# Optimization experiments

Hardware: AMD Instinct MI355X
Metric: run time of the kernel (lower is better)

## Reference

```python
import jax, jax.numpy as jnp
import numpy as np

N, E, D = 50000, 800000, 128   # nodes, edges, input feat dim
H, C = 4, 32                   # heads, per-head channels (H*C = 128)
OUT = 128                      # final linear out_channels
NEG_SLOPE = 0.2


def _glorot(k, shape):
    fan = shape[0] + shape[-1]
    return jax.random.normal(k, shape, jnp.float32) * np.float32(np.sqrt(2.0 / fan))


def setup_inputs() -> dict:
    key = jax.random.key(0)
    ks = jax.random.split(key, 16)
    HC = H * C
    z = lambda n: jnp.zeros((n,), jnp.float32)
    return {
        "x": jax.random.normal(ks[0], (N, D), jnp.float32),
        "edge_index": jax.random.randint(ks[1], (2, E), 0, N),
        "edge_attr": jax.random.uniform(ks[2], (E, 1), jnp.float32),
        # GATv2 layer 1 (in = D)
        "Wl1": _glorot(ks[3], (D, HC)), "bl1": z(HC),
        "Wr1": _glorot(ks[4], (D, HC)), "br1": z(HC),
        "We1": _glorot(ks[5], (1, HC)),
        "att1": _glorot(ks[6], (H, C)),
        "bo1": z(HC),
        # GATv2 layer 2 (in = H*C)
        "Wl2": _glorot(ks[7], (HC, HC)), "bl2": z(HC),
        "Wr2": _glorot(ks[8], (HC, HC)), "br2": z(HC),
        "We2": _glorot(ks[9], (1, HC)),
        "att2": _glorot(ks[10], (H, C)),
        "bo2": z(HC),
        # final Linear
        "Wlin": _glorot(ks[11], (HC, OUT)), "blin": z(OUT),
    }


def _segment_softmax(logits, seg, n):
    # logits: [E_tot, H], seg: [E_tot] target node ids
    m = jax.ops.segment_max(logits, seg, num_segments=n)          # [N, H]
    m = jnp.where(jnp.isfinite(m), m, 0.0)                         # empty-segment guard
    e = jnp.exp(logits - m[seg])
    s = jax.ops.segment_sum(e, seg, num_segments=n)                # [N, H]
    return e / (s[seg] + 1e-16)


def _gatv2_layer(x, src, dst, eattr, Wl, bl, Wr, br, We, att, bo):
    n = x.shape[0]
    xl = (x @ Wl + bl).reshape(n, H, C)   # source transform (lin_l)
    xr = (x @ Wr + br).reshape(n, H, C)   # target transform (lin_r)
    ee = (eattr @ We).reshape(-1, H, C)   # edge transform (lin_edge)
    m = jax.nn.leaky_relu(xl[src] + xr[dst] + ee, NEG_SLOPE)       # [E_tot, H, C]
    logits = jnp.einsum('ehc,hc->eh', m, att)                      # [E_tot, H]
    alpha = _segment_softmax(logits, dst, n)                       # [E_tot, H]
    out = jax.ops.segment_sum(xl[src] * alpha[..., None], dst, num_segments=n)
    return out.reshape(n, H * C) + bo


def _with_self_loops(edge_index, edge_attr, n):
    # PyG add_self_loops(fill_value='mean'): loop attr = mean of incoming edge attrs
    src, dst = edge_index[0], edge_index[1]
    sums = jax.ops.segment_sum(edge_attr, dst, num_segments=n)     # [N, 1]
    cnts = jax.ops.segment_sum(jnp.ones((edge_attr.shape[0], 1), edge_attr.dtype),
                               dst, num_segments=n)
    loop_attr = jnp.where(cnts > 0, sums / jnp.maximum(cnts, 1.0), 0.0)
    ar = jnp.arange(n, dtype=src.dtype)
    full_src = jnp.concatenate([src, ar])
    full_dst = jnp.concatenate([dst, ar])
    full_attr = jnp.concatenate([edge_attr, loop_attr], axis=0)
    return full_src, full_dst, full_attr


def reference(x, edge_index, edge_attr,
              Wl1, bl1, Wr1, br1, We1, att1, bo1,
              Wl2, bl2, Wr2, br2, We2, att2, bo2,
              Wlin, blin):
    x = x.astype(jnp.float32)
    edge_attr = edge_attr.astype(jnp.float32)
    src, dst, eattr = _with_self_loops(edge_index, edge_attr, x.shape[0])
    h = jax.nn.relu(_gatv2_layer(x, src, dst, eattr, Wl1, bl1, Wr1, br1, We1, att1, bo1))
    h = jax.nn.relu(_gatv2_layer(h, src, dst, eattr, Wl2, bl2, Wr2, br2, We2, att2, bo2))
    return jax.nn.relu(h @ Wlin + blin)
```

## Files before the change

kernel.cpp:

```cpp
#include <hip/hip_runtime.h>
#include <hip/hip_fp16.h>
#include <math.h>

#define NEG 0.2f
#define ROWS 48

typedef _Float16 hf2 __attribute__((ext_vector_type(2)));
typedef _Float16 hf8 __attribute__((ext_vector_type(8)));
typedef float f4 __attribute__((ext_vector_type(4)));

template <int CTRL>
__device__ __forceinline__ float dpp_radd(float x) {
  int t = __builtin_amdgcn_update_dpp(0, __float_as_int(x), CTRL, 0xf, 0xf,
                                      false);
  return x + __int_as_float(t);
}

__device__ __forceinline__ uint4 pack_wline(const float* __restrict__ W,
                                            int L) {
  int lane = L & 63, nt = (L >> 6) & 7, kc = L >> 9;
  int kbase = kc * 32 + (lane >> 4) * 8;
  int col = nt * 16 + (lane & 15);
  const float* wp = W + (size_t)kbase * 128 + col;
  uint4 pk;
  pk.x = __builtin_bit_cast(unsigned, __builtin_amdgcn_cvt_pkrtz(wp[0], wp[128]));
  pk.y = __builtin_bit_cast(unsigned, __builtin_amdgcn_cvt_pkrtz(wp[256], wp[384]));
  pk.z = __builtin_bit_cast(unsigned, __builtin_amdgcn_cvt_pkrtz(wp[512], wp[640]));
  pk.w = __builtin_bit_cast(unsigned, __builtin_amdgcn_cvt_pkrtz(wp[768], wp[896]));
  return pk;
}

__device__ __forceinline__ void load_batch(const unsigned* __restrict__ erow,
    int ofs, const hf2* __restrict__ xl, int lane, int n, unsigned* rec,
    hf2* xv) {
  const unsigned* ep = erow + ofs;
#pragma unroll
  for (int j = 0; j < 8; ++j) rec[j] = ep[j];
#pragma unroll
  for (int j = 0; j < 8; ++j) {
    unsigned si = rec[j] & 0xffffu;
    si = si < (unsigned)n ? si : 0u;
    xv[j] = xl[(size_t)si * 64 + lane];
  }
}

__device__ __forceinline__ void proc_batch(const unsigned* rec, const hf2* xv,
    int nvalid, hf2 xrh, hf2 weh, hf2 atth, hf2 negh, float* denom,
    float* ac0, float* ac1, float& easum) {
  float p[8];
#pragma unroll
  for (int j = 0; j < 8; ++j) {
    hf2 eah = __builtin_bit_cast(hf2, (rec[j] >> 16) * 0x10001u);
    easum += (j < nvalid) ? (float)eah.x : 0.f;
    hf2 t = (xv[j] + xrh) + eah * weh;
    hf2 tn = t * negh;
    t = __builtin_elementwise_max(t, tn);
    p[j] = __builtin_amdgcn_fdot2(t, atth, 0.f, false);
  }
#pragma unroll
  for (int j = 0; j < 8; ++j) {
    p[j] = dpp_radd<0xB1>(p[j]);
    p[j] = dpp_radd<0x4E>(p[j]);
    p[j] = dpp_radd<0x141>(p[j]);
    p[j] = dpp_radd<0x140>(p[j]);
  }
#pragma unroll
  for (int j = 0; j < 8; ++j) {
    float w = j < nvalid ? __builtin_amdgcn_exp2f(p[j]) : 0.f;
    denom[j & 1] += w;
    ac0[j & 1] = fmaf(w, (float)xv[j].x, ac0[j & 1]);
    ac1[j & 1] = fmaf(w, (float)xv[j].y, ac1[j & 1]);
  }
}

__device__ __forceinline__ hf2 gat_node(int v, const hf2* __restrict__ xl,
    const hf2* __restrict__ xr, const unsigned* __restrict__ edge,
    const unsigned* __restrict__ hist, hf2 weh, hf2 atth, hf2 negh,
    const float* __restrict__ bo, int lane, int n) {
  int ch = lane * 2;
  hf2 xrh = xr[(size_t)v * 64 + lane];
  int cnt = (int)hist[v];
  int cntc = cnt < ROWS ? cnt : ROWS;
  const unsigned* erow = edge + (size_t)v * ROWS;

  float denom[2] = {0.f, 0.f};
  float ac0[2] = {0.f, 0.f}, ac1[2] = {0.f, 0.f};
  float easum = 0.f;

  int nb = (cntc + 7) >> 3;
  if (nb > 0) {
    unsigned recA[8], recB[8];
    hf2 xvA[8], xvB[8];
    load_batch(erow, 0, xl, lane, n, recA, xvA);
    int b = 0;
    for (;;) {
      if (b + 1 < nb) {
        load_batch(erow, (b + 1) * 8, xl, lane, n, recB, xvB);
        proc_batch(recA, xvA, 8, xrh, weh, atth, negh, denom, ac0, ac1,
                   easum);
      } else {
        proc_batch(recA, xvA, cntc - b * 8, xrh, weh, atth, negh, denom, ac0,
                   ac1, easum);
        break;
      }
      ++b;
      if (b + 1 < nb) {
        load_batch(erow, (b + 1) * 8, xl, lane, n, recA, xvA);
        proc_batch(recB, xvB, 8, xrh, weh, atth, negh, denom, ac0, ac1,
                   easum);
      } else {
        proc_batch(recB, xvB, cntc - b * 8, xrh, weh, atth, negh, denom, ac0,
                   ac1, easum);
        break;
      }
      ++b;
    }
  }
  {
    float mean = cnt > 0 ? easum / (float)cnt : 0.f;
    hf2 xself = xl[(size_t)v * 64 + lane];
    _Float16 mh = (_Float16)mean;
    hf2 meanh = {mh, mh};
    hf2 t = (xself + xrh) + meanh * weh;
    hf2 tn = t * negh;
    t = __builtin_elementwise_max(t, tn);
    float ps = __builtin_amdgcn_fdot2(t, atth, 0.f, false);
    ps = dpp_radd<0xB1>(ps);
    ps = dpp_radd<0x4E>(ps);
    ps = dpp_radd<0x141>(ps);
    ps = dpp_radd<0x140>(ps);
    float w = __builtin_amdgcn_exp2f(ps);
    denom[0] += w;
    ac0[0] = fmaf(w, (float)xself.x, ac0[0]);
    ac1[0] = fmaf(w, (float)xself.y, ac1[0]);
  }
  float rden = 1.0f / (denom[0] + denom[1] + 1e-16f);
  int ch0 = ch;
  float o0 = fmaxf(fmaf(ac0[0] + ac0[1], rden, bo[ch0]), 0.f);
  float o1 = fmaxf(fmaf(ac1[0] + ac1[1], rden, bo[ch0 + 1]), 0.f);
  hf2 oh = {(_Float16)o0, (_Float16)o1};
  return oh;
}

__global__ __launch_bounds__(256) void k_csr(const int* __restrict__ ei,
    const float* __restrict__ eattr, unsigned* __restrict__ hist,
    unsigned* __restrict__ edge, int E) {
  int e0 = blockIdx.x * 1024 + threadIdx.x;
  int d[4], s[4];
  float ea[4];
  bool valid[4];
#pragma unroll
  for (int j = 0; j < 4; ++j) {
    int e = e0 + j * 256;
    valid[j] = e < E;
    int ec = valid[j] ? e : 0;
    d[j] = ei[E + ec];
    s[j] = ei[ec];
    ea[j] = eattr[ec];
  }
#pragma unroll
  for (int j = 0; j < 4; ++j) {
    if (valid[j]) {
      unsigned rank = atomicAdd(&hist[d[j]], 1u);
      _Float16 h = (_Float16)ea[j];
      unsigned hb = (unsigned)__builtin_bit_cast(unsigned short, h);
      if (rank < ROWS)
        edge[(size_t)d[j] * ROWS + rank] = (unsigned)s[j] | (hb << 16);
    }
  }
}

__global__ __launch_bounds__(256, 2) void k_fuse1(
    const float* __restrict__ X, const float* __restrict__ Wa,
    const float* __restrict__ Wb, const float* __restrict__ Ba,
    const float* __restrict__ Bb, hf2* __restrict__ Y0, hf2* __restrict__ Y1,
    int nrows, int gGemm,
    const float* __restrict__ W2a, const float* __restrict__ W2b,
    const float* __restrict__ W2c, uint4* __restrict__ wout) {
  __shared__ uint4 Wl[2][1024];
  int bid = blockIdx.x, tid = threadIdx.x;

  if (bid < gGemm) {
    int lane = tid & 63, wid = tid >> 6;
    int quad = lane >> 4, rl = lane & 15;
    int rbase = bid * 128 + wid * 32;

    hf8 a[4][2];
#pragma unroll
    for (int rs = 0; rs < 2; ++rs) {
      int gr = rbase + rs * 16 + rl;
      gr = gr < nrows ? gr : nrows - 1;
      const float* xp = X + (size_t)gr * 128 + quad * 8;
#pragma unroll
      for (int kc = 0; kc < 4; ++kc) {
        float4 u = *reinterpret_cast<const float4*>(xp + kc * 32);
        float4 u2 = *reinterpret_cast<const float4*>(xp + kc * 32 + 4);
        uint4 pk;
        pk.x = __builtin_bit_cast(unsigned, __builtin_amdgcn_cvt_pkrtz(u.x, u.y));
        pk.y = __builtin_bit_cast(unsigned, __builtin_amdgcn_cvt_pkrtz(u.z, u.w));
        pk.z = __builtin_bit_cast(unsigned, __builtin_amdgcn_cvt_pkrtz(u2.x, u2.y));
        pk.w = __builtin_bit_cast(unsigned, __builtin_amdgcn_cvt_pkrtz(u2.z, u2.w));
        a[kc][rs] = __builtin_bit_cast(hf8, pk);
      }
    }

    f4 acc[2][2][8];
#pragma unroll
    for (int m = 0; m < 2; ++m)
#pragma unroll
      for (int rs = 0; rs < 2; ++rs)
#pragma unroll
        for (int nt = 0; nt < 8; ++nt) acc[m][rs][nt] = (f4)0.f;

#pragma unroll
    for (int h = 0; h < 2; ++h) {
      __syncthreads();
#pragma unroll
      for (int m = 0; m < 2; ++m) {
        const float* W = m ? Wb : Wa;
        for (int i = tid; i < 1024; i += 256)
          Wl[m][i] = pack_wline(W, h * 1024 + i);
      }
      __syncthreads();
#pragma unroll
      for (int kcl = 0; kcl < 2; ++kcl) {
        int kc = h * 2 + kcl;
#pragma unroll
        for (int nt = 0; nt < 8; ++nt) {
#pragma unroll
          for (int m = 0; m < 2; ++m) {
            hf8 w = __builtin_bit_cast(hf8,
                Wl[m][(kcl * 8 + nt) * 64 + lane]);
            acc[m][0][nt] = __builtin_amdgcn_mfma_f32_16x16x32_f16(
                w, a[kc][0], acc[m][0][nt], 0, 0, 0);
            acc[m][1][nt] = __builtin_amdgcn_mfma_f32_16x16x32_f16(
                w, a[kc][1], acc[m][1][nt], 0, 0, 0);
          }
        }
      }
    }

#pragma unroll
    for (int m = 0; m < 2; ++m) {
      const float* Bb_ = m ? Bb : Ba;
      hf2* Yv = m ? Y1 : Y0;
#pragma unroll
      for (int rs = 0; rs < 2; ++rs) {
        int row = rbase + rs * 16 + rl;
        if (row < nrows) {
#pragma unroll
          for (int nt = 0; nt < 8; ++nt) {
            f4 av = acc[m][rs][nt];
            int col = nt * 16 + quad * 4;
            float4 bb = *reinterpret_cast<const float4*>(&Bb_[col]);
            float o0 = av[0] + bb.x, o1 = av[1] + bb.y;
            float o2 = av[2] + bb.z, o3 = av[3] + bb.w;
            unsigned p0 = __builtin_bit_cast(unsigned,
                __builtin_amdgcn_cvt_pkrtz(o0, o1));
            unsigned p1 = __builtin_bit_cast(unsigned,
                __builtin_amdgcn_cvt_pkrtz(o2, o3));
            *reinterpret_cast<uint2*>((_Float16*)Yv + (size_t)row * 128 + col)
                = make_uint2(p0, p1);
          }
        }
      }
    }
  } else {
    int gid = (bid - gGemm) * 256 + tid;
    if (gid < 3 * 2048) {
      int mat = gid >> 11;
      const float* W = mat == 0 ? W2a : mat == 1 ? W2b : W2c;
      wout[gid] = pack_wline(W, gid & 2047);
    }
  }
}

__global__ __launch_bounds__(256) void k_gatg(const hf2* __restrict__ xl,
    const hf2* __restrict__ xr, const unsigned* __restrict__ edge,
    const unsigned* __restrict__ hist, const float* __restrict__ We,
    const float* __restrict__ att, const float* __restrict__ bo,
    const uint4* __restrict__ Wp0, const uint4* __restrict__ Wp1,
    const float* __restrict__ B0, const float* __restrict__ B1,
    hf2* __restrict__ out0, hf2* __restrict__ out1, int n) {
  __shared__ _Float16 hbuf[16][136];
  int tid = threadIdx.x;
  int lane = tid & 63, wid = tid >> 6;
  int quad = lane >> 4, rl = lane & 15;
  int base = blockIdx.x * 16;
  int ch = lane * 2;
  hf2 weh = {(_Float16)We[ch], (_Float16)We[ch + 1]};
  hf2 atth = {(_Float16)(att[ch] * 1.44269504f),
              (_Float16)(att[ch + 1] * 1.44269504f)};
  hf2 negh = {(_Float16)NEG, (_Float16)NEG};

#pragma unroll 1
  for (int i = 0; i < 4; ++i) {
    int row = wid * 4 + i;
    int v = base + row;
    hf2 oh = {(_Float16)0.f, (_Float16)0.f};
    if (v < n)
      oh = gat_node(__builtin_amdgcn_readfirstlane(v), xl, xr, edge, hist,
                    weh, atth, negh, bo, lane, n);
    *reinterpret_cast<hf2*>(&hbuf[row][2 * lane]) = oh;
  }
  __syncthreads();

  hf8 hfrag[4];
#pragma unroll
  for (int kc = 0; kc < 4; ++kc)
    hfrag[kc] = *reinterpret_cast<const hf8*>(&hbuf[rl][kc * 32 + quad * 8]);

#pragma unroll
  for (int ntl = 0; ntl < 2; ++ntl) {
    int nt = wid * 2 + ntl;
#pragma unroll
    for (int m = 0; m < 2; ++m) {
      const uint4* Wp = m ? Wp1 : Wp0;
      f4 a = (f4)0.f;
#pragma unroll
      for (int kc = 0; kc < 4; ++kc) {
        hf8 w = __builtin_bit_cast(hf8, Wp[(kc * 8 + nt) * 64 + lane]);
        a = __builtin_amdgcn_mfma_f32_16x16x32_f16(w, hfrag[kc], a, 0, 0, 0);
      }
      int col = nt * 16 + quad * 4;
      const float* Bb = m ? B1 : B0;
      float4 bb = *reinterpret_cast<const float4*>(&Bb[col]);
      float o0 = a[0] + bb.x, o1 = a[1] + bb.y;
      float o2 = a[2] + bb.z, o3 = a[3] + bb.w;
      hf2 h0 = {(_Float16)o0, (_Float16)o1};
      hf2 h1 = {(_Float16)o2, (_Float16)o3};
      int row = base + rl;
      if (row < n) {
        hf2* outp = m ? out1 : out0;
        uint2 pk = make_uint2(__builtin_bit_cast(unsigned, h0),
                              __builtin_bit_cast(unsigned, h1));
        *reinterpret_cast<uint2*>(outp + (size_t)row * 64 + nt * 8 + quad * 2)
            = pk;
      }
    }
  }
}

__global__ __launch_bounds__(256) void k_gatf(const hf2* __restrict__ xl,
    const hf2* __restrict__ xr, const unsigned* __restrict__ edge,
    const unsigned* __restrict__ hist, const float* __restrict__ We,
    const float* __restrict__ att, const float* __restrict__ bo,
    const uint4* __restrict__ Wp, const float* __restrict__ Blin,
    float* __restrict__ out, int n) {
  __shared__ _Float16 hbuf[16][136];
  int tid = threadIdx.x;
  int lane = tid & 63, wid = tid >> 6;
  int quad = lane >> 4, rl = lane & 15;
  int base = blockIdx.x * 16;
  int ch = lane * 2;
  hf2 weh = {(_Float16)We[ch], (_Float16)We[ch + 1]};
  hf2 atth = {(_Float16)(att[ch] * 1.44269504f),
              (_Float16)(att[ch + 1] * 1.44269504f)};
  hf2 negh = {(_Float16)NEG, (_Float16)NEG};

#pragma unroll 1
  for (int i = 0; i < 4; ++i) {
    int row = wid * 4 + i;
    int v = base + row;
    hf2 oh = {(_Float16)0.f, (_Float16)0.f};
    if (v < n)
      oh = gat_node(__builtin_amdgcn_readfirstlane(v), xl, xr, edge, hist,
                    weh, atth, negh, bo, lane, n);
    *reinterpret_cast<hf2*>(&hbuf[row][2 * lane]) = oh;
  }
  __syncthreads();

  hf8 hfrag[4];
#pragma unroll
  for (int kc = 0; kc < 4; ++kc)
    hfrag[kc] = *reinterpret_cast<const hf8*>(&hbuf[rl][kc * 32 + quad * 8]);

  int row = base + rl;
#pragma unroll
  for (int ntl = 0; ntl < 2; ++ntl) {
    int nt = wid * 2 + ntl;
    f4 a = (f4)0.f;
#pragma unroll
    for (int kc = 0; kc < 4; ++kc) {
      hf8 w = __builtin_bit_cast(hf8, Wp[(kc * 8 + nt) * 64 + lane]);
      a = __builtin_amdgcn_mfma_f32_16x16x32_f16(w, hfrag[kc], a, 0, 0, 0);
    }
    int col = nt * 16 + quad * 4;
    float4 bb = *reinterpret_cast<const float4*>(&Blin[col]);
    if (row < n) {
      float o0 = fmaxf(a[0] + bb.x, 0.f);
      float o1 = fmaxf(a[1] + bb.y, 0.f);
      float o2 = fmaxf(a[2] + bb.z, 0.f);
      float o3 = fmaxf(a[3] + bb.w, 0.f);
      *reinterpret_cast<float4*>(&out[(size_t)row * 128 + col]) =
          make_float4(o0, o1, o2, o3);
    }
  }
}

__global__ __launch_bounds__(256) void k_gat(const hf2* __restrict__ xl,
    const hf2* __restrict__ xr, const unsigned* __restrict__ edge,
    const unsigned* __restrict__ hist, const float* __restrict__ We,
    const float* __restrict__ att, const float* __restrict__ bo,
    hf2* __restrict__ out, int n) {
  int lane = threadIdx.x & 63;
  int wid = threadIdx.x >> 6;
  int v = blockIdx.x * 4 + wid;
  if (v >= n) return;
  int ch = lane * 2;
  hf2 weh = {(_Float16)We[ch], (_Float16)We[ch + 1]};
  hf2 atth = {(_Float16)(att[ch] * 1.44269504f),
              (_Float16)(att[ch + 1] * 1.44269504f)};
  hf2 negh = {(_Float16)NEG, (_Float16)NEG};
  hf2 oh = gat_node(__builtin_amdgcn_readfirstlane(v), xl, xr, edge, hist,
                    weh, atth, negh, bo, lane, n);
  out[(size_t)v * 64 + lane] = oh;
}

__global__ __launch_bounds__(256, 2) void k_gemmf(
    const _Float16* __restrict__ X, const uint4* __restrict__ Wp0,
    const float* __restrict__ B0, float* __restrict__ Y, int nrows) {
  __shared__ uint4 Wl[2048];
  int tid = threadIdx.x;
  for (int i = tid; i < 2048; i += 256) Wl[i] = Wp0[i];

  int lane = tid & 63, wid = tid >> 6;
  int quad = lane >> 4, rl = lane & 15;
  int rbase = blockIdx.x * 128 + wid * 32;

  hf8 a[4][2];
#pragma unroll
  for (int rs = 0; rs < 2; ++rs) {
    int gr = rbase + rs * 16 + rl;
    gr = gr < nrows ? gr : nrows - 1;
    const _Float16* xp = X + (size_t)gr * 128 + quad * 8;
#pragma unroll
    for (int kc = 0; kc < 4; ++kc)
      a[kc][rs] = *reinterpret_cast<const hf8*>(xp + kc * 32);
  }

  f4 acc[2][8];
#pragma unroll
  for (int rs = 0; rs < 2; ++rs)
#pragma unroll
    for (int nt = 0; nt < 8; ++nt) acc[rs][nt] = (f4)0.f;

  __syncthreads();

#pragma unroll
  for (int kc = 0; kc < 4; ++kc) {
#pragma unroll
    for (int nt = 0; nt < 8; ++nt) {
      hf8 w = __builtin_bit_cast(hf8, Wl[(kc * 8 + nt) * 64 + lane]);
      acc[0][nt] = __builtin_amdgcn_mfma_f32_16x16x32_f16(
          w, a[kc][0], acc[0][nt], 0, 0, 0);
      acc[1][nt] = __builtin_amdgcn_mfma_f32_16x16x32_f16(
          w, a[kc][1], acc[1][nt], 0, 0, 0);
    }
  }

#pragma unroll
  for (int rs = 0; rs < 2; ++rs) {
    int row = rbase + rs * 16 + rl;
    if (row < nrows) {
#pragma unroll
      for (int nt = 0; nt < 8; ++nt) {
        f4 av = acc[rs][nt];
        int col = nt * 16 + quad * 4;
        float4 bb = *reinterpret_cast<const float4*>(&B0[col]);
        float o0 = fmaxf(av[0] + bb.x, 0.f);
        float o1 = fmaxf(av[1] + bb.y, 0.f);
        float o2 = fmaxf(av[2] + bb.z, 0.f);
        float o3 = fmaxf(av[3] + bb.w, 0.f);
        *reinterpret_cast<float4*>(&Y[(size_t)row * 128 + col]) =
            make_float4(o0, o1, o2, o3);
      }
    }
  }
}

extern "C" void kernel_launch(void* const* d_in, const int* in_sizes, int n_in,
                              void* d_out, int out_size, void* d_ws, size_t ws_size,
                              hipStream_t stream) {
  const float* x     = (const float*)d_in[0];
  const int*   ei    = (const int*)d_in[1];
  const float* eattr = (const float*)d_in[2];
  const float* Wl1 = (const float*)d_in[3];
  const float* bl1 = (const float*)d_in[4];
  const float* Wr1 = (const float*)d_in[5];
  const float* br1 = (const float*)d_in[6];
  const float* We1 = (const float*)d_in[7];
  const float* att1 = (const float*)d_in[8];
  const float* bo1 = (const float*)d_in[9];
  const float* Wl2 = (const float*)d_in[10];
  const float* bl2 = (const float*)d_in[11];
  const float* Wr2 = (const float*)d_in[12];
  const float* br2 = (const float*)d_in[13];
  const float* We2 = (const float*)d_in[14];
  const float* att2 = (const float*)d_in[15];
  const float* bo2 = (const float*)d_in[16];
  const float* Wlin = (const float*)d_in[17];
  const float* blin = (const float*)d_in[18];
  float* out = (float*)d_out;

  const int N = in_sizes[0] / 128;
  const int E = in_sizes[1] / 2;

  hf2* xl = (hf2*)d_ws;
  hf2* xr = xl + (size_t)N * 64;
  hf2* h16 = xr + (size_t)N * 64;
  uint4* w16 = (uint4*)(h16 + (size_t)N * 64);
  unsigned* hist = (unsigned*)(w16 + 3 * 2048);
  unsigned* edge = hist + N;
  hf2* xr2w = (hf2*)(edge + (size_t)N * ROWS);

  size_t need_fused = (size_t)N * 256 * 4 + 3 * 2048 * 16 +
                      (size_t)N * 4 + (size_t)N * ROWS * 4;
  bool fused34 = ws_size >= need_fused;

  (void)hipMemsetAsync(hist, 0, sizeof(unsigned) * (size_t)N, stream);

  int gGemm = (N + 127) / 128;
  int gCsr = (E + 1023) / 1024;
  int gGat = (N + 3) / 4;
  int gGatg = (N + 15) / 16;

  k_csr<<<gCsr, 256, 0, stream>>>(ei, eattr, hist, edge, E);

  k_fuse1<<<gGemm + 24, 256, 0, stream>>>(x, Wl1, Wr1, bl1, br1,
      xl, xr, N, gGemm, Wl2, Wr2, Wlin, w16);

  if (fused34) {
    hf2* xl2 = h16;
    hf2* xr2 = xr2w;
    k_gatg<<<gGatg, 256, 0, stream>>>(xl, xr, edge, hist, We1, att1, bo1,
        w16, w16 + 2048, bl2, br2, xl2, xr2, N);
    k_gatf<<<gGatg, 256, 0, stream>>>(xl2, xr2, edge, hist, We2, att2, bo2,
        w16 + 2 * 2048, blin, out, N);
  } else {
    hf2* xl2 = (hf2*)d_out;
    hf2* xr2 = xl2 + (size_t)N * 64;
    k_gatg<<<gGatg, 256, 0, stream>>>(xl, xr, edge, hist, We1, att1, bo1,
        w16, w16 + 2048, bl2, br2, xl2, xr2, N);
    k_gat<<<gGat, 256, 0, stream>>>(xl2, xr2, edge, hist, We2, att2, bo2,
                                    h16, N);
    k_gemmf<<<gGemm, 256, 0, stream>>>((const _Float16*)h16, w16 + 2 * 2048,
                                       blin, out, N);
  }
}
```

Before: 276.5 us.

## Fuse all stages into one persistent kernel with software grid barriers

Replaces the four-kernel sequence (CSR build, first GEMM, two GAT layers) with a single persistent kernel of a fixed block count. Phases are separated by a two-level atomic grid barrier, and work is distributed with grid-stride task loops. The first GEMM now uses 64-row tiles, and CSR tasks process 16 edges per thread. This removes launch gaps and tail effects between kernels, but it relies on all 1024 blocks being co-resident, otherwise the barrier deadlocks, and it adds barrier spin overhead and occupancy limits from launch_bounds(256,4).

```diff
diff --git a/kernel.cpp b/kernel.cpp
--- a/kernel.cpp
+++ b/kernel.cpp
@@ -4,6 +4,7 @@
 
 #define NEG 0.2f
 #define ROWS 48
+#define NBLK 1024
 
 typedef _Float16 hf2 __attribute__((ext_vector_type(2)));
 typedef _Float16 hf8 __attribute__((ext_vector_type(8)));
@@ -28,6 +29,25 @@
   pk.z = __builtin_bit_cast(unsigned, __builtin_amdgcn_cvt_pkrtz(wp[512], wp[640]));
   pk.w = __builtin_bit_cast(unsigned, __builtin_amdgcn_cvt_pkrtz(wp[768], wp[896]));
   return pk;
+}
+
+__device__ __forceinline__ void gbar(unsigned* bar, unsigned phase) {
+  __syncthreads();
+  if (threadIdx.x == 0) {
+    __threadfence();
+    unsigned lv = atomicAdd(&bar[blockIdx.x & 63], 1u) + 1;
+    if (lv == phase * (NBLK / 64)) {
+      unsigned rv = atomicAdd(&bar[64], 1u) + 1;
+      if (rv == phase * 64)
+        __hip_atomic_store(&bar[65], phase, __ATOMIC_RELEASE,
+                           __HIP_MEMORY_SCOPE_AGENT);
+    }
+    while (__hip_atomic_load(&bar[65], __ATOMIC_ACQUIRE,
+                             __HIP_MEMORY_SCOPE_AGENT) < phase)
+      __builtin_amdgcn_s_sleep(2);
+    __threadfence();
+  }
+  __syncthreads();
 }
 
 __device__ __forceinline__ void load_batch(const unsigned* __restrict__ erow,
@@ -142,6 +162,288 @@
   return oh;
 }
 
+
+__device__ __forceinline__ void gemm64(int task, const float* __restrict__ X,
+    const float* __restrict__ Wa, const float* __restrict__ Wb,
+    const float* __restrict__ Ba, const float* __restrict__ Bb,
+    hf2* __restrict__ Y0, hf2* __restrict__ Y1, int nrows,
+    uint4 (*wl)[1024], int tid) {
+  int lane = tid & 63, wid = tid >> 6;
+  int quad = lane >> 4, rl = lane & 15;
+  int rbase = task * 64 + wid * 16;
+  int gr = rbase + rl;
+  gr = gr < nrows ? gr : nrows - 1;
+
+  hf8 a[4];
+  const float* xp = X + (size_t)gr * 128 + quad * 8;
+#pragma unroll
+  for (int kc = 0; kc < 4; ++kc) {
+    float4 u = *reinterpret_cast<const float4*>(xp + kc * 32);
+    float4 u2 = *reinterpret_cast<const float4*>(xp + kc * 32 + 4);
+    uint4 pk;
+    pk.x = __builtin_bit_cast(unsigned, __builtin_amdgcn_cvt_pkrtz(u.x, u.y));
+    pk.y = __builtin_bit_cast(unsigned, __builtin_amdgcn_cvt_pkrtz(u.z, u.w));
+    pk.z = __builtin_bit_cast(unsigned, __builtin_amdgcn_cvt_pkrtz(u2.x, u2.y));
+    pk.w = __builtin_bit_cast(unsigned, __builtin_amdgcn_cvt_pkrtz(u2.z, u2.w));
+    a[kc] = __builtin_bit_cast(hf8, pk);
+  }
+
+  f4 acc[2][8];
+#pragma unroll
+  for (int m = 0; m < 2; ++m)
+#pragma unroll
+    for (int nt = 0; nt < 8; ++nt) acc[m][nt] = (f4)0.f;
+
+#pragma unroll
+  for (int h = 0; h < 2; ++h) {
+    __syncthreads();
+#pragma unroll
+    for (int m = 0; m < 2; ++m) {
+      const float* W = m ? Wb : Wa;
+      for (int i = tid; i < 1024; i += 256)
+        wl[m][i] = pack_wline(W, h * 1024 + i);
+    }
+    __syncthreads();
+#pragma unroll
+    for (int kcl = 0; kcl < 2; ++kcl) {
+      int kc = h * 2 + kcl;
+#pragma unroll
+      for (int nt = 0; nt < 8; ++nt) {
+#pragma unroll
+        for (int m = 0; m < 2; ++m) {
+          hf8 w = __builtin_bit_cast(hf8, wl[m][(kcl * 8 + nt) * 64 + lane]);
+          acc[m][nt] = __builtin_amdgcn_mfma_f32_16x16x32_f16(
+              w, a[kc], acc[m][nt], 0, 0, 0);
+        }
+      }
+    }
+  }
+
+  int row = rbase + rl;
+  if (row < nrows) {
+#pragma unroll
+    for (int m = 0; m < 2; ++m) {
+      const float* Bb_ = m ? Bb : Ba;
+      hf2* Yv = m ? Y1 : Y0;
+#pragma unroll
+      for (int nt = 0; nt < 8; ++nt) {
+        f4 av = acc[m][nt];
+        int col = nt * 16 + quad * 4;
+        float4 bb = *reinterpret_cast<const float4*>(&Bb_[col]);
+        float o0 = av[0] + bb.x, o1 = av[1] + bb.y;
+        float o2 = av[2] + bb.z, o3 = av[3] + bb.w;
+        unsigned p0 = __builtin_bit_cast(unsigned,
+            __builtin_amdgcn_cvt_pkrtz(o0, o1));
+        unsigned p1 = __builtin_bit_cast(unsigned,
+            __builtin_amdgcn_cvt_pkrtz(o2, o3));
+        *reinterpret_cast<uint2*>((_Float16*)Yv + (size_t)row * 128 + col) =
+            make_uint2(p0, p1);
+      }
+    }
+  }
+}
+
+__device__ __forceinline__ void csr16(int cb, const int* __restrict__ ei,
+    const float* __restrict__ eattr, unsigned* __restrict__ hist,
+    unsigned* __restrict__ edge, int E, int tid) {
+  int e0 = cb * 4096 + tid;
+  int d[16], s[16];
+  float ea[16];
+  bool valid[16];
+#pragma unroll
+  for (int j = 0; j < 16; ++j) {
+    int e = e0 + j * 256;
+    valid[j] = e < E;
+    int ec = valid[j] ? e : 0;
+    d[j] = ei[E + ec];
+    s[j] = ei[ec];
+    ea[j] = eattr[ec];
+  }
+#pragma unroll
+  for (int j = 0; j < 16; ++j) {
+    if (valid[j]) {
+      unsigned rank = atomicAdd(&hist[d[j]], 1u);
+      _Float16 h = (_Float16)ea[j];
+      unsigned hb = (unsigned)__builtin_bit_cast(unsigned short, h);
+      if (rank < ROWS)
+        edge[(size_t)d[j] * ROWS + rank] = (unsigned)s[j] | (hb << 16);
+    }
+  }
+}
+
+__device__ __forceinline__ void tile_gatg(int t, _Float16 (*hb)[136],
+    const hf2* __restrict__ xl, const hf2* __restrict__ xr,
+    const unsigned* __restrict__ edge, const unsigned* __restrict__ hist,
+    hf2 weh, hf2 atth, hf2 negh, const float* __restrict__ bo,
+    const uint4* __restrict__ Wp0, const uint4* __restrict__ Wp1,
+    const float* __restrict__ B0, const float* __restrict__ B1,
+    hf2* __restrict__ out0, hf2* __restrict__ out1, int n, int tid) {
+  int lane = tid & 63, wid = tid >> 6;
+  int quad = lane >> 4, rl = lane & 15;
+  int base = t * 16;
+#pragma unroll 1
+  for (int i = 0; i < 4; ++i) {
+    int row = wid * 4 + i;
+    int v = base + row;
+    hf2 oh = {(_Float16)0.f, (_Float16)0.f};
+    if (v < n)
+      oh = gat_node(__builtin_amdgcn_readfirstlane(v), xl, xr, edge, hist,
+                    weh, atth, negh, bo, lane, n);
+    *reinterpret_cast<hf2*>(&hb[row][2 * lane]) = oh;
+  }
+  __syncthreads();
+
+  hf8 hfrag[4];
+#pragma unroll
+  for (int kc = 0; kc < 4; ++kc)
+    hfrag[kc] = *reinterpret_cast<const hf8*>(&hb[rl][kc * 32 + quad * 8]);
+
+#pragma unroll
+  for (int ntl = 0; ntl < 2; ++ntl) {
+    int nt = wid * 2 + ntl;
+#pragma unroll
+    for (int m = 0; m < 2; ++m) {
+      const uint4* Wp = m ? Wp1 : Wp0;
+      f4 a = (f4)0.f;
+#pragma unroll
+      for (int kc = 0; kc < 4; ++kc) {
+        hf8 w = __builtin_bit_cast(hf8, Wp[(kc * 8 + nt) * 64 + lane]);
+        a = __builtin_amdgcn_mfma_f32_16x16x32_f16(w, hfrag[kc], a, 0, 0, 0);
+      }
+      int col = nt * 16 + quad * 4;
+      const float* Bb = m ? B1 : B0;
+      float4 bb = *reinterpret_cast<const float4*>(&Bb[col]);
+      float o0 = a[0] + bb.x, o1 = a[1] + bb.y;
+      float o2 = a[2] + bb.z, o3 = a[3] + bb.w;
+      hf2 h0 = {(_Float16)o0, (_Float16)o1};
+      hf2 h1 = {(_Float16)o2, (_Float16)o3};
+      int row = base + rl;
+      if (row < n) {
+        hf2* outp = m ? out1 : out0;
+        uint2 pk = make_uint2(__builtin_bit_cast(unsigned, h0),
+                              __builtin_bit_cast(unsigned, h1));
+        *reinterpret_cast<uint2*>(outp + (size_t)row * 64 + nt * 8 + quad * 2)
+            = pk;
+      }
+    }
+  }
+  __syncthreads();
+}
+
+__device__ __forceinline__ void tile_gatf(int t, _Float16 (*hb)[136],
+    const hf2* __restrict__ xl, const hf2* __restrict__ xr,
+    const unsigned* __restrict__ edge, const unsigned* __restrict__ hist,
+    hf2 weh, hf2 atth, hf2 negh, const float* __restrict__ bo,
+    const uint4* __restrict__ Wp, const float* __restrict__ Blin,
+    float* __restrict__ out, int n, int tid) {
+  int lane = tid & 63, wid = tid >> 6;
+  int quad = lane >> 4, rl = lane & 15;
+  int base = t * 16;
+#pragma unroll 1
+  for (int i = 0; i < 4; ++i) {
+    int row = wid * 4 + i;
+    int v = base + row;
+    hf2 oh = {(_Float16)0.f, (_Float16)0.f};
+    if (v < n)
+      oh = gat_node(__builtin_amdgcn_readfirstlane(v), xl, xr, edge, hist,
+                    weh, atth, negh, bo, lane, n);
+    *reinterpret_cast<hf2*>(&hb[row][2 * lane]) = oh;
+  }
+  __syncthreads();
+
+  hf8 hfrag[4];
+#pragma unroll
+  for (int kc = 0; kc < 4; ++kc)
+    hfrag[kc] = *reinterpret_cast<const hf8*>(&hb[rl][kc * 32 + quad * 8]);
+
+  int row = base + rl;
+#pragma unroll
+  for (int ntl = 0; ntl < 2; ++ntl) {
+    int nt = wid * 2 + ntl;
+    f4 a = (f4)0.f;
+#pragma unroll
+    for (int kc = 0; kc < 4; ++kc) {
+      hf8 w = __builtin_bit_cast(hf8, Wp[(kc * 8 + nt) * 64 + lane]);
+      a = __builtin_amdgcn_mfma_f32_16x16x32_f16(w, hfrag[kc], a, 0, 0, 0);
+    }
+    int col = nt * 16 + quad * 4;
+    float4 bb = *reinterpret_cast<const float4*>(&Blin[col]);
+    if (row < n) {
+      float o0 = fmaxf(a[0] + bb.x, 0.f);
+      float o1 = fmaxf(a[1] + bb.y, 0.f);
+      float o2 = fmaxf(a[2] + bb.z, 0.f);
+      float o3 = fmaxf(a[3] + bb.w, 0.f);
+      *reinterpret_cast<float4*>(&out[(size_t)row * 128 + col]) =
+          make_float4(o0, o1, o2, o3);
+    }
+  }
+  __syncthreads();
+}
+
+__global__ __launch_bounds__(256, 4) void k_mega(
+    const float* __restrict__ X, const float* __restrict__ Wa,
+    const float* __restrict__ Wb, const float* __restrict__ Ba,
+    const float* __restrict__ Bb, hf2* __restrict__ xl, hf2* __restrict__ xr,
+    int nrows, int gG64, const int* __restrict__ ei,
+    const float* __restrict__ eattr, unsigned* __restrict__ hist,
+    unsigned* __restrict__ edge, int E, int nbP,
+    const float* __restrict__ W2a, const float* __restrict__ W2b,
+    const float* __restrict__ W2c, uint4* __restrict__ w16,
+    const float* __restrict__ We1, const float* __restrict__ att1,
+    const float* __restrict__ bo1, const float* __restrict__ bl2,
+    const float* __restrict__ br2, hf2* __restrict__ xl2,
+    hf2* __restrict__ xr2, const float* __restrict__ We2,
+    const float* __restrict__ att2, const float* __restrict__ bo2,
+    const float* __restrict__ blin, float* __restrict__ out, int n,
+    int gTile, unsigned* __restrict__ bar) {
+  __shared__ union SM {
+    uint4 wl[2][1024];
+    _Float16 hb[16][136];
+  } sm;
+  int tid = threadIdx.x, bid = blockIdx.x;
+  int lane = tid & 63;
+  int ch = lane * 2;
+
+  int totT = gG64 + nbP + 24;
+  for (int task = bid; task < totT; task += NBLK) {
+    if (task < gG64) {
+      gemm64(task, X, Wa, Wb, Ba, Bb, xl, xr, nrows, sm.wl, tid);
+    } else if (task < gG64 + nbP) {
+      csr16(task - gG64, ei, eattr, hist, edge, E, tid);
+    } else {
+      int gid = (task - gG64 - nbP) * 256 + tid;
+      if (gid < 3 * 2048) {
+        int mat = gid >> 11;
+        const float* W = mat == 0 ? W2a : mat == 1 ? W2b : W2c;
+        w16[gid] = pack_wline(W, gid & 2047);
+      }
+    }
+  }
+  gbar(bar, 1);
+
+  {
+    hf2 weh = {(_Float16)We1[ch], (_Float16)We1[ch + 1]};
+    hf2 atth = {(_Float16)(att1[ch] * 1.44269504f),
+                (_Float16)(att1[ch + 1] * 1.44269504f)};
+    hf2 negh = {(_Float16)NEG, (_Float16)NEG};
+    for (int t = bid; t < gTile; t += NBLK)
+      tile_gatg(t, sm.hb, xl, xr, edge, hist, weh, atth, negh, bo1,
+                w16, w16 + 2048, bl2, br2, xl2, xr2, n, tid);
+  }
+  gbar(bar, 2);
+
+  {
+    hf2 weh = {(_Float16)We2[ch], (_Float16)We2[ch + 1]};
+    hf2 atth = {(_Float16)(att2[ch] * 1.44269504f),
+                (_Float16)(att2[ch + 1] * 1.44269504f)};
+    hf2 negh = {(_Float16)NEG, (_Float16)NEG};
+    for (int t = bid; t < gTile; t += NBLK)
+      tile_gatf(t, sm.hb, xl2, xr2, edge, hist, weh, atth, negh, bo2,
+                w16 + 2 * 2048, blin, out, n, tid);
+  }
+}
+
+
 __global__ __launch_bounds__(256) void k_csr(const int* __restrict__ ei,
     const float* __restrict__ eattr, unsigned* __restrict__ hist,
     unsigned* __restrict__ edge, int E) {
@@ -229,8 +531,7 @@
         for (int nt = 0; nt < 8; ++nt) {
 #pragma unroll
           for (int m = 0; m < 2; ++m) {
-            hf8 w = __builtin_bit_cast(hf8,
-                Wl[m][(kcl * 8 + nt) * 64 + lane]);
+            hf8 w = __builtin_bit_cast(hf8, Wl[m][(kcl * 8 + nt) * 64 + lane]);
             acc[m][0][nt] = __builtin_amdgcn_mfma_f32_16x16x32_f16(
                 w, a[kc][0], acc[m][0][nt], 0, 0, 0);
             acc[m][1][nt] = __builtin_amdgcn_mfma_f32_16x16x32_f16(
@@ -284,61 +585,14 @@
     hf2* __restrict__ out0, hf2* __restrict__ out1, int n) {
   __shared__ _Float16 hbuf[16][136];
   int tid = threadIdx.x;
-  int lane = tid & 63, wid = tid >> 6;
-  int quad = lane >> 4, rl = lane & 15;
-  int base = blockIdx.x * 16;
+  int lane = tid & 63;
   int ch = lane * 2;
   hf2 weh = {(_Float16)We[ch], (_Float16)We[ch + 1]};
   hf2 atth = {(_Float16)(att[ch] * 1.44269504f),
               (_Float16)(att[ch + 1] * 1.44269504f)};
   hf2 negh = {(_Float16)NEG, (_Float16)NEG};
-
-#pragma unroll 1
-  for (int i = 0; i < 4; ++i) {
-    int row = wid * 4 + i;
-    int v = base + row;
-    hf2 oh = {(_Float16)0.f, (_Float16)0.f};
-    if (v < n)
-      oh = gat_node(__builtin_amdgcn_readfirstlane(v), xl, xr, edge, hist,
-                    weh, atth, negh, bo, lane, n);
-    *reinterpret_cast<hf2*>(&hbuf[row][2 * lane]) = oh;
-  }
-  __syncthreads();
-
-  hf8 hfrag[4];
-#pragma unroll
-  for (int kc = 0; kc < 4; ++kc)
-    hfrag[kc] = *reinterpret_cast<const hf8*>(&hbuf[rl][kc * 32 + quad * 8]);
-
-#pragma unroll
-  for (int ntl = 0; ntl < 2; ++ntl) {
-    int nt = wid * 2 + ntl;
-#pragma unroll
-    for (int m = 0; m < 2; ++m) {
-      const uint4* Wp = m ? Wp1 : Wp0;
-      f4 a = (f4)0.f;
-#pragma unroll
-      for (int kc = 0; kc < 4; ++kc) {
-        hf8 w = __builtin_bit_cast(hf8, Wp[(kc * 8 + nt) * 64 + lane]);
-        a = __builtin_amdgcn_mfma_f32_16x16x32_f16(w, hfrag[kc], a, 0, 0, 0);
-      }
-      int col = nt * 16 + quad * 4;
-      const float* Bb = m ? B1 : B0;
-      float4 bb = *reinterpret_cast<const float4*>(&Bb[col]);
-      float o0 = a[0] + bb.x, o1 = a[1] + bb.y;
-      float o2 = a[2] + bb.z, o3 = a[3] + bb.w;
-      hf2 h0 = {(_Float16)o0, (_Float16)o1};
-      hf2 h1 = {(_Float16)o2, (_Float16)o3};
-      int row = base + rl;
-      if (row < n) {
-        hf2* outp = m ? out1 : out0;
-        uint2 pk = make_uint2(__builtin_bit_cast(unsigned, h0),
-                              __builtin_bit_cast(unsigned, h1));
-        *reinterpret_cast<uint2*>(outp + (size_t)row * 64 + nt * 8 + quad * 2)
-            = pk;
-      }
-    }
-  }
+  tile_gatg(blockIdx.x, hbuf, xl, xr, edge, hist, weh, atth, negh, bo,
+            Wp0, Wp1, B0, B1, out0, out1, n, tid);
 }
 
 __global__ __launch_bounds__(256) void k_gatf(const hf2* __restrict__ xl,
@@ -349,134 +603,14 @@
     float* __restrict__ out, int n) {
   __shared__ _Float16 hbuf[16][136];
   int tid = threadIdx.x;
-  int lane = tid & 63, wid = tid >> 6;
-  int quad = lane >> 4, rl = lane & 15;
-  int base = blockIdx.x * 16;
+  int lane = tid & 63;
   int ch = lane * 2;
   hf2 weh = {(_Float16)We[ch], (_Float16)We[ch + 1]};
   hf2 atth = {(_Float16)(att[ch] * 1.44269504f),
               (_Float16)(att[ch + 1] * 1.44269504f)};
   hf2 negh = {(_Float16)NEG, (_Float16)NEG};
-
-#pragma unroll 1
-  for (int i = 0; i < 4; ++i) {
-    int row = wid * 4 + i;
-    int v = base + row;
-    hf2 oh = {(_Float16)0.f, (_Float16)0.f};
-    if (v < n)
-      oh = gat_node(__builtin_amdgcn_readfirstlane(v), xl, xr, edge, hist,
-                    weh, atth, negh, bo, lane, n);
-    *reinterpret_cast<hf2*>(&hbuf[row][2 * lane]) = oh;
-  }
-  __syncthreads();
-
-  hf8 hfrag[4];
-#pragma unroll
-  for (int kc = 0; kc < 4; ++kc)
-    hfrag[kc] = *reinterpret_cast<const hf8*>(&hbuf[rl][kc * 32 + quad * 8]);
-
-  int row = base + rl;
-#pragma unroll
-  for (int ntl = 0; ntl < 2; ++ntl) {
-    int nt = wid * 2 + ntl;
-    f4 a = (f4)0.f;
-#pragma unroll
-    for (int kc = 0; kc < 4; ++kc) {
-      hf8 w = __builtin_bit_cast(hf8, Wp[(kc * 8 + nt) * 64 + lane]);
-      a = __builtin_amdgcn_mfma_f32_16x16x32_f16(w, hfrag[kc], a, 0, 0, 0);
-    }
-    int col = nt * 16 + quad * 4;
-    float4 bb = *reinterpret_cast<const float4*>(&Blin[col]);
-    if (row < n) {
-      float o0 = fmaxf(a[0] + bb.x, 0.f);
-      float o1 = fmaxf(a[1] + bb.y, 0.f);
-      float o2 = fmaxf(a[2] + bb.z, 0.f);
-      float o3 = fmaxf(a[3] + bb.w, 0.f);
-      *reinterpret_cast<float4*>(&out[(size_t)row * 128 + col]) =
-          make_float4(o0, o1, o2, o3);
-    }
-  }
-}
-
-__global__ __launch_bounds__(256) void k_gat(const hf2* __restrict__ xl,
-    const hf2* __restrict__ xr, const unsigned* __restrict__ edge,
-    const unsigned* __restrict__ hist, const float* __restrict__ We,
-    const float* __restrict__ att, const float* __restrict__ bo,
-    hf2* __restrict__ out, int n) {
-  int lane = threadIdx.x & 63;
-  int wid = threadIdx.x >> 6;
-  int v = blockIdx.x * 4 + wid;
-  if (v >= n) return;
-  int ch = lane * 2;
-  hf2 weh = {(_Float16)We[ch], (_Float16)We[ch + 1]};
-  hf2 atth = {(_Float16)(att[ch] * 1.44269504f),
-              (_Float16)(att[ch + 1] * 1.44269504f)};
-  hf2 negh = {(_Float16)NEG, (_Float16)NEG};
-  hf2 oh = gat_node(__builtin_amdgcn_readfirstlane(v), xl, xr, edge, hist,
-                    weh, atth, negh, bo, lane, n);
-  out[(size_t)v * 64 + lane] = oh;
-}
-
-__global__ __launch_bounds__(256, 2) void k_gemmf(
-    const _Float16* __restrict__ X, const uint4* __restrict__ Wp0,
-    const float* __restrict__ B0, float* __restrict__ Y, int nrows) {
-  __shared__ uint4 Wl[2048];
-  int tid = threadIdx.x;
-  for (int i = tid; i < 2048; i += 256) Wl[i] = Wp0[i];
-
-  int lane = tid & 63, wid = tid >> 6;
-  int quad = lane >> 4, rl = lane & 15;
-  int rbase = blockIdx.x * 128 + wid * 32;
-
-  hf8 a[4][2];
-#pragma unroll
-  for (int rs = 0; rs < 2; ++rs) {
-    int gr = rbase + rs * 16 + rl;
-    gr = gr < nrows ? gr : nrows - 1;
-    const _Float16* xp = X + (size_t)gr * 128 + quad * 8;
-#pragma unroll
-    for (int kc = 0; kc < 4; ++kc)
-      a[kc][rs] = *reinterpret_cast<const hf8*>(xp + kc * 32);
-  }
-
-  f4 acc[2][8];
-#pragma unroll
-  for (int rs = 0; rs < 2; ++rs)
-#pragma unroll
-    for (int nt = 0; nt < 8; ++nt) acc[rs][nt] = (f4)0.f;
-
-  __syncthreads();
-
-#pragma unroll
-  for (int kc = 0; kc < 4; ++kc) {
-#pragma unroll
-    for (int nt = 0; nt < 8; ++nt) {
-      hf8 w = __builtin_bit_cast(hf8, Wl[(kc * 8 + nt) * 64 + lane]);
-      acc[0][nt] = __builtin_amdgcn_mfma_f32_16x16x32_f16(
-          w, a[kc][0], acc[0][nt], 0, 0, 0);
-      acc[1][nt] = __builtin_amdgcn_mfma_f32_16x16x32_f16(
-          w, a[kc][1], acc[1][nt], 0, 0, 0);
-    }
-  }
-
-#pragma unroll
-  for (int rs = 0; rs < 2; ++rs) {
-    int row = rbase + rs * 16 + rl;
-    if (row < nrows) {
-#pragma unroll
-      for (int nt = 0; nt < 8; ++nt) {
-        f4 av = acc[rs][nt];
-        int col = nt * 16 + quad * 4;
-        float4 bb = *reinterpret_cast<const float4*>(&B0[col]);
-        float o0 = fmaxf(av[0] + bb.x, 0.f);
-        float o1 = fmaxf(av[1] + bb.y, 0.f);
-        float o2 = fmaxf(av[2] + bb.z, 0.f);
-        float o3 = fmaxf(av[3] + bb.w, 0.f);
-        *reinterpret_cast<float4*>(&Y[(size_t)row * 128 + col]) =
-            make_float4(o0, o1, o2, o3);
-      }
-    }
-  }
+  tile_gatf(blockIdx.x, hbuf, xl, xr, edge, hist, weh, atth, negh, bo,
+            Wp, Blin, out, n, tid);
 }
 
 extern "C" void kernel_launch(void* const* d_in, const int* in_sizes, int n_in,
@@ -506,45 +640,41 @@
   const int N = in_sizes[0] / 128;
   const int E = in_sizes[1] / 2;
 
+  const size_t xb = (size_t)N * 256;
+  const size_t w16b = 3 * 2048 * 16;
+  const size_t edgeb = (size_t)N * ROWS * 4;
+
   hf2* xl = (hf2*)d_ws;
   hf2* xr = xl + (size_t)N * 64;
-  hf2* h16 = xr + (size_t)N * 64;
-  uint4* w16 = (uint4*)(h16 + (size_t)N * 64);
+  hf2* xl2 = xr + (size_t)N * 64;
+  uint4* w16 = (uint4*)(xl2 + (size_t)N * 64);
   unsigned* hist = (unsigned*)(w16 + 3 * 2048);
-  unsigned* edge = hist + N;
-  hf2* xr2w = (hf2*)(edge + (size_t)N * ROWS);
-
-  size_t need_fused = (size_t)N * 256 * 4 + 3 * 2048 * 16 +
-                      (size_t)N * 4 + (size_t)N * ROWS * 4;
-  bool fused34 = ws_size >= need_fused;
-
-  (void)hipMemsetAsync(hist, 0, sizeof(unsigned) * (size_t)N, stream);
-
-  int gGemm = (N + 127) / 128;
-  int gCsr = (E + 1023) / 1024;
-  int gGat = (N + 3) / 4;
-  int gGatg = (N + 15) / 16;
-
-  k_csr<<<gCsr, 256, 0, stream>>>(ei, eattr, hist, edge, E);
-
-  k_fuse1<<<gGemm + 24, 256, 0, stream>>>(x, Wl1, Wr1, bl1, br1,
-      xl, xr, N, gGemm, Wl2, Wr2, Wlin, w16);
-
-  if (fused34) {
-    hf2* xl2 = h16;
-    hf2* xr2 = xr2w;
-    k_gatg<<<gGatg, 256, 0, stream>>>(xl, xr, edge, hist, We1, att1, bo1,
+  unsigned* bar = hist + N;
+  unsigned* edge = bar + 128;
+  hf2* xr2 = (hf2*)(edge + (size_t)N * ROWS);
+
+  size_t need = 4 * xb + w16b + (size_t)N * 4 + 512 + edgeb;
+  int gG64 = (N + 63) / 64;
+  int nbP = (E + 4095) / 4096;
+  int gTile = (N + 15) / 16;
+  bool mega = ws_size >= need && (gG64 + nbP + 24) > 0;
+
+  if (mega) {
+    (void)hipMemsetAsync(hist, 0, sizeof(unsigned) * (size_t)N + 512, stream);
+    k_mega<<<NBLK, 256, 0, stream>>>(x, Wl1, Wr1, bl1, br1, xl, xr, N, gG64,
+        ei, eattr, hist, edge, E, nbP, Wl2, Wr2, Wlin, w16,
+        We1, att1, bo1, bl2, br2, xl2, xr2, We2, att2, bo2, blin, out, N,
+        gTile, bar);
+  } else {
+    (void)hipMemsetAsync(hist, 0, sizeof(unsigned) * (size_t)N, stream);
+    int gGemm = (N + 127) / 128;
+    int gCsr = (E + 1023) / 1024;
+    k_csr<<<gCsr, 256, 0, stream>>>(ei, eattr, hist, edge, E);
+    k_fuse1<<<gGemm + 24, 256, 0, stream>>>(x, Wl1, Wr1, bl1, br1,
+        xl, xr, N, gGemm, Wl2, Wr2, Wlin, w16);
+    k_gatg<<<gTile, 256, 0, stream>>>(xl, xr, edge, hist, We1, att1, bo1,
         w16, w16 + 2048, bl2, br2, xl2, xr2, N);
-    k_gatf<<<gGatg, 256, 0, stream>>>(xl2, xr2, edge, hist, We2, att2, bo2,
+    k_gatf<<<gTile, 256, 0, stream>>>(xl2, xr2, edge, hist, We2, att2, bo2,
         w16 + 2 * 2048, blin, out, N);
-  } else {
-    hf2* xl2 = (hf2*)d_out;
-    hf2* xr2 = xl2 + (size_t)N * 64;
-    k_gatg<<<gGatg, 256, 0, stream>>>(xl, xr, edge, hist, We1, att1, bo1,
-        w16, w16 + 2048, bl2, br2, xl2, xr2, N);
-    k_gat<<<gGat, 256, 0, stream>>>(xl2, xr2, edge, hist, We2, att2, bo2,
-                                    h16, N);
-    k_gemmf<<<gGemm, 256, 0, stream>>>((const _Float16*)h16, w16 + 2 * 2048,
-                                       blin, out, N);
-  }
-}
+  }
+}
```

New measurement: 775.6 us. 181% more time.
